# Performance work log

Hardware: AMD Instinct MI355X
Metric: run time of the kernel (lower is better)

## Reference

```python
import jax, jax.numpy as jnp
import numpy as np

B, SEQ, D = 4, 1024, 1024
H = 16
HD = D // H            # 64, matches cos/sin last dim
S_COLS, TOPK = 8, 2
INTER = 768            # find_multiple(round(1.0 * D * 2 / 3), 256)
EPS = 1e-5


def setup_inputs() -> dict:
    key = jax.random.key(0)
    ks = jax.random.split(key, 6)
    hidden_states = jax.random.normal(ks[0], (B, SEQ, D), jnp.float32)
    # RoPE tables (standard rotary, theta=10000)
    inv_freq = 1.0 / (10000.0 ** (jnp.arange(0, HD, 2, dtype=jnp.float32) / HD))
    freqs = jnp.outer(jnp.arange(SEQ, dtype=jnp.float32), inv_freq)
    emb = jnp.concatenate([freqs, freqs], axis=-1)  # [SEQ, HD]
    cos, sin = jnp.cos(emb), jnp.sin(emb)
    Wr = jax.random.normal(ks[1], (S_COLS, D), jnp.float32) * 0.02
    temperature = jnp.ones((1,), jnp.float32)
    # Stacked per-column TransformerBlock params (bias-free linears)
    Wqkv = jax.random.normal(ks[2], (S_COLS, D, 3 * D), jnp.float32) * 0.02
    Wo = jax.random.normal(ks[3], (S_COLS, D, D), jnp.float32) * 0.02
    Wgu = jax.random.normal(ks[4], (S_COLS, D, 2 * INTER), jnp.float32) * 0.02
    Wd = jax.random.normal(ks[5], (S_COLS, INTER, D), jnp.float32) * 0.02
    return dict(hidden_states=hidden_states, cos=cos, sin=sin, Wr=Wr,
                temperature=temperature, Wqkv=Wqkv, Wo=Wo, Wgu=Wgu, Wd=Wd)


def _rms_norm(x):
    return x * jax.lax.rsqrt(jnp.mean(x * x, axis=-1, keepdims=True) + EPS)


def _rotate_half(x):
    x1, x2 = jnp.split(x, 2, axis=-1)
    return jnp.concatenate([-x2, x1], axis=-1)


def _columns_forward(x, Wqkv, Wo, Wgu, Wd, cos, sin):
    # x: [n, seq, D] dispatched sequences; params gathered per dispatch entry [n, ...]
    n, seq, d = x.shape
    qkv = jnp.einsum('nsd,nde->nse', x, Wqkv)
    q, k, v = jnp.split(qkv, 3, axis=-1)
    q = q.reshape(n, seq, H, HD)
    k = k.reshape(n, seq, H, HD)
    v = v.reshape(n, seq, H, HD)
    c = cos[None, :, None, :]
    s = sin[None, :, None, :]
    q = q * c + _rotate_half(q) * s
    k = k * c + _rotate_half(k) * s
    scores = jnp.einsum('nqhd,nkhd->nhqk', q, k) / jnp.sqrt(jnp.asarray(HD, x.dtype))
    attn = jax.nn.softmax(scores, axis=-1)  # non-causal (HRM-style block)
    ctx = jnp.einsum('nhqk,nkhd->nqhd', attn, v).reshape(n, seq, d)
    attn_out = jnp.einsum('nsd,nde->nse', ctx, Wo)
    x = _rms_norm(x + attn_out)                      # post-norm residual
    gu = jnp.einsum('nsd,nde->nse', x, Wgu)
    gate, up = jnp.split(gu, 2, axis=-1)
    mlp_out = jnp.einsum('nsi,nid->nsd', jax.nn.silu(gate) * up, Wd)
    return _rms_norm(x + mlp_out)


def reference(hidden_states, cos, sin, Wr, temperature, Wqkv, Wo, Wgu, Wd):
    Bn = hidden_states.shape[0]
    temp = jnp.clip(temperature, 0.1, 10.0)
    routing_logits = (hidden_states.mean(axis=1) @ Wr.T) / temp   # [B, S]
    topk_vals, topk_idx = jax.lax.top_k(routing_logits, TOPK)
    weights = jax.nn.softmax(topk_vals, axis=-1)                  # [B, k]
    flat_idx = topk_idx.reshape(-1)                               # [B*k] expert ids
    flat_w = weights.reshape(-1)
    sample_idx = jnp.repeat(jnp.arange(Bn), TOPK)                 # [B*k]
    # Sparse dispatch: exactly B*k block forwards via per-entry param gather
    x_disp = hidden_states[sample_idx]
    col_out = _columns_forward(x_disp, Wqkv[flat_idx], Wo[flat_idx],
                               Wgu[flat_idx], Wd[flat_idx], cos, sin)
    result = jnp.zeros_like(hidden_states).at[sample_idx].add(
        flat_w[:, None, None] * col_out)
    return result, routing_logits
```

## Files before the change

### kernel.cpp

```cpp
#include <hip/hip_runtime.h>
#include <hip/hip_bf16.h>
#include <math.h>

#define B_     4
#define SEQ_   1024
#define D_     1024
#define H_     16
#define NE_    8
#define INTER_ 768
#define EPS_   1e-5f

typedef unsigned short u16;
typedef __attribute__((ext_vector_type(8))) short s8v;
typedef __attribute__((ext_vector_type(4))) short s4v;
typedef __attribute__((ext_vector_type(4))) float f4v;
typedef __attribute__((ext_vector_type(4))) unsigned short u16x4;
typedef __attribute__((ext_vector_type(8))) unsigned short u16x8;

__device__ __forceinline__ u16 f2bf(float x) {
    union { float f; unsigned u; } c; c.f = x;
    unsigned r = (c.u + 0x7FFFu + ((c.u >> 16) & 1u)) >> 16;
    return (u16)r;
}
__device__ __forceinline__ float bf2f(u16 h) {
    union { unsigned u; float f; } c; c.u = ((unsigned)h) << 16;
    return c.f;
}
__device__ __forceinline__ unsigned pk2(float a, float b) {
    union { float f; unsigned u; } x, y; x.f = a; y.f = b;
    return ((x.u + 0x8000u) >> 16) | ((y.u + 0x8000u) & 0xffff0000u);
}

#define GLDS16(gp, lp) \
    __builtin_amdgcn_global_load_lds((const __attribute__((address_space(1))) unsigned int*)(gp), \
                                     (__attribute__((address_space(3))) unsigned int*)(lp), 16, 0, 0)

__global__ void route1(const float* __restrict__ hidden, float* __restrict__ part,
                       u16* __restrict__ hb) {
    int b = blockIdx.x, ch = blockIdx.y, t = threadIdx.x;
    const float* xb = hidden + (size_t)b * SEQ_ * D_ + (size_t)ch * 32 * D_;
    u16* ho = hb + (size_t)b * SEQ_ * D_ + (size_t)ch * 32 * D_;
    float4 acc = make_float4(0.f, 0.f, 0.f, 0.f);
    for (int r = 0; r < 32; ++r) {
        float4 v = *(const float4*)&xb[(size_t)r * D_ + t * 4];
        acc.x += v.x; acc.y += v.y; acc.z += v.z; acc.w += v.w;
        u16x4 o = {f2bf(v.x), f2bf(v.y), f2bf(v.z), f2bf(v.w)};
        *(u16x4*)&ho[(size_t)r * D_ + t * 4] = o;
    }
    *(float4*)&part[((size_t)(b * 32 + ch)) * D_ + t * 4] = acc;
}

__global__ void route2(const float* __restrict__ part, const float* __restrict__ Wr,
                       const float* __restrict__ temp, float* __restrict__ out_logits,
                       int* __restrict__ flat_idx, float* __restrict__ flat_w) {
    __shared__ float col[1024];
    __shared__ float sm[8];
    int b = blockIdx.x, t = threadIdx.x;
    float4 s = make_float4(0.f, 0.f, 0.f, 0.f);
    for (int ch = 0; ch < 32; ++ch) {
        float4 v = *(const float4*)&part[((size_t)(b * 32 + ch)) * D_ + t * 4];
        s.x += v.x; s.y += v.y; s.z += v.z; s.w += v.w;
    }
    col[t * 4 + 0] = s.x * (1.f / 1024.f);
    col[t * 4 + 1] = s.y * (1.f / 1024.f);
    col[t * 4 + 2] = s.z * (1.f / 1024.f);
    col[t * 4 + 3] = s.w * (1.f / 1024.f);
    __syncthreads();
    int j = t >> 5, d0 = t & 31;
    float p = 0.f;
    for (int d = d0; d < 1024; d += 32) p += col[d] * Wr[j * 1024 + d];
    for (int off = 16; off >= 1; off >>= 1) p += __shfl_down(p, off, 32);
    if (d0 == 0) sm[j] = p;
    __syncthreads();
    if (t == 0) {
        float tc = temp[0];
        tc = fminf(fmaxf(tc, 0.1f), 10.0f);
        float lg[8];
        for (int jj = 0; jj < 8; ++jj) {
            lg[jj] = sm[jj] / tc;
            out_logits[b * 8 + jj] = lg[jj];
        }
        int i0 = 0; float v0 = lg[0];
        for (int jj = 1; jj < 8; ++jj) if (lg[jj] > v0) { v0 = lg[jj]; i0 = jj; }
        int i1 = -1; float v1 = -1e30f;
        for (int jj = 0; jj < 8; ++jj) if (jj != i0 && lg[jj] > v1) { v1 = lg[jj]; i1 = jj; }
        float e1 = expf(v1 - v0);
        flat_idx[2 * b]     = i0;
        flat_idx[2 * b + 1] = i1;
        flat_w[2 * b]       = 1.0f / (1.0f + e1);
        flat_w[2 * b + 1]   = e1 / (1.0f + e1);
    }
}

__global__ __launch_bounds__(256) void wtrans_all(const float* __restrict__ Wqkv,
                                                  const float* __restrict__ Wo,
                                                  const float* __restrict__ Wgu,
                                                  const float* __restrict__ Wd,
                                                  u16* __restrict__ WqkvT, u16* __restrict__ WoT,
                                                  u16* __restrict__ WguT, u16* __restrict__ WdT) {
    int bid = blockIdx.x;
    const float* W; u16* Wt; int K, N, nx, gu = 0;
    if (bid < 6144)      { W = Wqkv; Wt = WqkvT; K = 1024; N = 3072; nx = 48; }
    else if (bid < 8192) { bid -= 6144;  W = Wo;  Wt = WoT;  K = 1024; N = 1024; nx = 16; }
    else if (bid < 11264){ bid -= 8192;  W = Wgu; Wt = WguT; K = 1024; N = 1536; nx = 24; gu = 1; }
    else                 { bid -= 11264; W = Wd;  Wt = WdT;  K = 768;  N = 1024; nx = 16; }
    int x = bid % nx; bid /= nx;
    int ny = K >> 6;
    int y = bid % ny;
    int e = bid / ny;

    __shared__ float tile[64][65];
    int k0 = y * 64, n0 = x * 64;
    const float* Wp = W + (size_t)e * K * N;
    u16* Wtp = Wt + (size_t)e * K * N;
    int t = threadIdx.x;
    int kk = t >> 4, ns = t & 15;
#pragma unroll
    for (int p = 0; p < 4; ++p) {
        float4 v = *(const float4*)&Wp[(size_t)(k0 + kk + p * 16) * N + n0 + ns * 4];
        tile[kk + p * 16][ns * 4 + 0] = v.x;
        tile[kk + p * 16][ns * 4 + 1] = v.y;
        tile[kk + p * 16][ns * 4 + 2] = v.z;
        tile[kk + p * 16][ns * 4 + 3] = v.w;
    }
    __syncthreads();
    int nn = t >> 3, ks = t & 7;
#pragma unroll
    for (int p = 0; p < 2; ++p) {
        int n = n0 + nn + p * 32;
        int nd = n;
        if (gu) nd = (n < 768) ? ((n >> 4) << 5) + (n & 15)
                               : (((n - 768) >> 4) << 5) + 16 + (n & 15);
        u16x8 o;
#pragma unroll
        for (int jj = 0; jj < 8; ++jj) o[jj] = f2bf(tile[ks * 8 + jj][nn + p * 32]);
        *(u16x8*)&Wtp[(size_t)nd * K + k0 + ks * 8] = o;
    }
}

#define GEMM_CORE(A, Wt, K)                                                                 \
    f4v acc[4][4];                                                                          \
    _Pragma("unroll") for (int i = 0; i < 4; ++i)                                           \
        _Pragma("unroll") for (int jj = 0; jj < 4; ++jj) acc[i][jj] = (f4v){0.f,0.f,0.f,0.f}; \
    for (int k0 = 0; k0 < K; k0 += 32) {                                                    \
        _Pragma("unroll") for (int it = 0; it < 2; ++it) {                                  \
            int p = it * 256 + w * 64 + lane;                                               \
            int row = p >> 2, seg = (p & 3) ^ ((row >> 1) & 3);                             \
            GLDS16(A  + (size_t)(m0 + row) * K + k0 + seg * 8, As + (size_t)(it*256 + w*64) * 8); \
            GLDS16(Wt + (size_t)(n0 + row) * K + k0 + seg * 8, Bs + (size_t)(it*256 + w*64) * 8); \
        }                                                                                   \
        __syncthreads();                                                                    \
        s8v af[4], bfr[4];                                                                  \
        _Pragma("unroll") for (int ti = 0; ti < 4; ++ti) {                                  \
            int r = wm + ti * 16 + c;                                                       \
            af[ti]  = *(const s8v*)&As[r * 32 + (g ^ ((r >> 1) & 3)) * 8];                   \
        }                                                                                   \
        _Pragma("unroll") for (int tj = 0; tj < 4; ++tj) {                                  \
            int r = wn + tj * 16 + c;                                                       \
            bfr[tj] = *(const s8v*)&Bs[r * 32 + (g ^ ((r >> 1) & 3)) * 8];                   \
        }                                                                                   \
        _Pragma("unroll") for (int ti = 0; ti < 4; ++ti)                                    \
            _Pragma("unroll") for (int tj = 0; tj < 4; ++tj)                                \
                acc[ti][tj] = __builtin_amdgcn_mfma_f32_16x16x32_bf16(af[ti], bfr[tj], acc[ti][tj], 0, 0, 0); \
        __syncthreads();                                                                    \
    }

__global__ __launch_bounds__(256) void gemm_bf16(const u16* __restrict__ Abase,
                                                 const u16* __restrict__ Wtbase,
                                                 u16* __restrict__ Cb,
                                                 const int* __restrict__ flat_idx,
                                                 int M, int N, int K, int aDiv) {
    __shared__ __align__(16) u16 As[128 * 32];
    __shared__ __align__(16) u16 Bs[128 * 32];
    int e = blockIdx.z;
    const u16* A  = Abase + (size_t)(e / aDiv) * M * K;
    const u16* Wt = Wtbase + (size_t)flat_idx[e] * N * K;
    int m0 = blockIdx.y * 128, n0 = blockIdx.x * 128;
    int t = threadIdx.x, lane = t & 63, w = t >> 6;
    int g = lane >> 4, c = lane & 15;
    int wm = (w >> 1) * 64, wn = (w & 1) * 64;

    GEMM_CORE(A, Wt, K)

    u16* C = Cb + (size_t)e * M * N;
#pragma unroll
    for (int ti = 0; ti < 4; ++ti)
#pragma unroll
        for (int tj = 0; tj < 4; ++tj)
#pragma unroll
            for (int i = 0; i < 4; ++i)
                C[(size_t)(m0 + wm + ti * 16 + g * 4 + i) * N + n0 + wn + tj * 16 + c] = f2bf(acc[ti][tj][i]);
}

__global__ __launch_bounds__(256) void gemm_qkv(const u16* __restrict__ Abase,
                                                const u16* __restrict__ Wtbase,
                                                const int* __restrict__ flat_idx,
                                                const float* __restrict__ cosb,
                                                const float* __restrict__ sinb,
                                                u16* __restrict__ Qb, u16* __restrict__ Kb,
                                                u16* __restrict__ Vb) {
    __shared__ __align__(16) u16 As[128 * 32];
    __shared__ __align__(16) u16 Bs[128 * 32];
    const int K = 1024, N = 3072;
    int e = blockIdx.z;
    const u16* A  = Abase + (size_t)(e >> 1) * 1024 * K;
    const u16* Wt = Wtbase + (size_t)flat_idx[e] * N * K;
    int m0 = blockIdx.y * 128, n0 = blockIdx.x * 128;
    int t = threadIdx.x, lane = t & 63, w = t >> 6;
    int g = lane >> 4, c = lane & 15;
    int wm = (w >> 1) * 64, wn = (w & 1) * 64;

    GEMM_CORE(A, Wt, K)

    int col0 = n0 + wn;
    int sb = m0 + wm + g * 4;
    if (col0 < 2048) {
        bool isq = col0 < 1024;
        u16* dst = isq ? Qb : Kb;
        int h = (col0 & 1023) >> 6;
        const float scl = isq ? 0.125f * 1.44269504f : 1.0f;
#pragma unroll
        for (int ti = 0; ti < 4; ++ti)
#pragma unroll
            for (int i = 0; i < 4; ++i) {
                int s = sb + ti * 16 + i;
                size_t ob = ((size_t)(e * 1024) + s) * 1024 + h * 64;
#pragma unroll
                for (int tj = 0; tj < 2; ++tj) {
                    int d = tj * 16 + c;
                    float x1 = acc[ti][tj][i], x2 = acc[ti][tj + 2][i];
                    float c1 = cosb[s * 64 + d],      s1 = sinb[s * 64 + d];
                    float c2 = cosb[s * 64 + d + 32], s2 = sinb[s * 64 + d + 32];
                    dst[ob + d]      = f2bf((x1 * c1 - x2 * s1) * scl);
                    dst[ob + d + 32] = f2bf((x2 * c2 + x1 * s2) * scl);
                }
            }
    } else {
        int vcol = col0 - 2048;
#pragma unroll
        for (int ti = 0; ti < 4; ++ti)
#pragma unroll
            for (int tj = 0; tj < 4; ++tj)
#pragma unroll
                for (int i = 0; i < 4; ++i)
                    Vb[((size_t)(e * 1024) + sb + ti * 16 + i) * 1024 + vcol + tj * 16 + c] = f2bf(acc[ti][tj][i]);
    }
}

__global__ __launch_bounds__(256) void gemm_wgu_silu(const u16* __restrict__ Abase,
                                                     const u16* __restrict__ Wtbase,
                                                     u16* __restrict__ act,
                                                     const int* __restrict__ flat_idx) {
    __shared__ __align__(16) u16 As[128 * 32];
    __shared__ __align__(16) u16 Bs[128 * 32];
    const int K = 1024, N = 1536;
    int e = blockIdx.z;
    const u16* A  = Abase + (size_t)e * 1024 * K;
    const u16* Wt = Wtbase + (size_t)flat_idx[e] * N * K;
    int m0 = blockIdx.y * 128, n0 = blockIdx.x * 128;
    int t = threadIdx.x, lane = t & 63, w = t >> 6;
    int g = lane >> 4, c = lane & 15;
    int wm = (w >> 1) * 64, wn = (w & 1) * 64;

    GEMM_CORE(A, Wt, K)

    int col0 = n0 + wn;
    int oc0 = (col0 >> 1) + c;
    int sb = m0 + wm + g * 4;
#pragma unroll
    for (int ti = 0; ti < 4; ++ti)
#pragma unroll
        for (int i = 0; i < 4; ++i) {
            size_t rb = ((size_t)(e * 1024) + sb + ti * 16 + i) * 768;
#pragma unroll
            for (int pr = 0; pr < 2; ++pr) {
                float gt = acc[ti][pr * 2][i];
                float up = acc[ti][pr * 2 + 1][i];
                act[rb + oc0 + pr * 16] = f2bf(gt / (1.f + __expf(-gt)) * up);
            }
        }
}

__global__ __launch_bounds__(256) void vtrans(const u16* __restrict__ Vb, u16* __restrict__ Vtg) {
    __shared__ __align__(16) u16 tile[64 * 72];
    int s0 = blockIdx.x * 64;
    int eh = blockIdx.y;
    int e = eh >> 4, h = eh & 15;
    int t = threadIdx.x;
#pragma unroll
    for (int it = 0; it < 2; ++it) {
        int p = it * 256 + t;
        int sr = p >> 3, ds = p & 7;
        u16x8 v = *(const u16x8*)&Vb[((size_t)(e * 1024) + s0 + sr) * 1024 + h * 64 + ds * 8];
        *(u16x8*)&tile[sr * 72 + ds * 8] = v;
    }
    __syncthreads();
#pragma unroll
    for (int it = 0; it < 2; ++it) {
        int p = it * 256 + t;
        int d = p >> 3, ks = p & 7;
        u16x8 o;
#pragma unroll
        for (int jj = 0; jj < 8; ++jj) o[jj] = tile[(ks * 8 + jj) * 72 + d];
        *(u16x8*)&Vtg[((size_t)((e * 16 + h) * 64) + d) * 1024 + s0 + ks * 8] = o;
    }
}

__global__ __launch_bounds__(256) void attn_mfma(const u16* __restrict__ Qb, const u16* __restrict__ Kb,
                                                 const u16* __restrict__ Vtg, u16* __restrict__ ctx) {
    __shared__ __align__(16) u16 Ks[64 * 64];
    __shared__ __align__(16) u16 Vt[64 * 64];
    int e = blockIdx.x, h = blockIdx.y, qt = blockIdx.z;
    int t = threadIdx.x, lane = t & 63, w = t >> 6;
    int g = lane >> 4, c = lane & 15;
    int q0 = qt * 64 + w * 16;

    s8v qf[2];
#pragma unroll
    for (int ks = 0; ks < 2; ++ks)
        qf[ks] = *(const s8v*)&Qb[((size_t)(e * 1024) + q0 + c) * 1024 + h * 64 + ks * 32 + g * 8];

    f4v O[4];
#pragma unroll
    for (int tj = 0; tj < 4; ++tj) O[tj] = (f4v){0.f, 0.f, 0.f, 0.f};
    f4v liacc = (f4v){0.f, 0.f, 0.f, 0.f};
    const s4v vone = {(short)0x3F80, (short)0x3F80, (short)0x3F80, (short)0x3F80};

    for (int kt = 0; kt < 16; ++kt) {
#pragma unroll
        for (int it = 0; it < 2; ++it) {
            int p = it * 256 + w * 64 + lane;
            int row = p >> 3, ss = p & 7;
            GLDS16(Kb + ((size_t)(e * 1024 + kt * 64 + row)) * 1024 + h * 64 + (ss ^ (row & 7)) * 8,
                   Ks + (size_t)(it * 256 + w * 64) * 8);
            GLDS16(Vtg + ((size_t)((e * 16 + h) * 64 + row)) * 1024 + kt * 64 + (ss ^ (row & 7)) * 8,
                   Vt + (size_t)(it * 256 + w * 64) * 8);
        }
        __syncthreads();

        f4v st[4];
#pragma unroll
        for (int tj = 0; tj < 4; ++tj) st[tj] = (f4v){0.f, 0.f, 0.f, 0.f};
#pragma unroll
        for (int ks = 0; ks < 2; ++ks)
#pragma unroll
            for (int tj = 0; tj < 4; ++tj) {
                int kvl = tj * 16 + c;
                s8v kf = *(const s8v*)&Ks[kvl * 64 + (((ks * 4 + g) ^ (kvl & 7)) * 8)];
                st[tj] = __builtin_amdgcn_mfma_f32_16x16x32_bf16(kf, qf[ks], st[tj], 0, 0, 0);
            }

        s4v pf[4];
#pragma unroll
        for (int tj = 0; tj < 4; ++tj) {
            float p0 = __builtin_amdgcn_exp2f(st[tj][0]);
            float p1 = __builtin_amdgcn_exp2f(st[tj][1]);
            float p2 = __builtin_amdgcn_exp2f(st[tj][2]);
            float p3 = __builtin_amdgcn_exp2f(st[tj][3]);
            union { unsigned u[2]; s4v v; } pu;
            pu.u[0] = pk2(p0, p1);
            pu.u[1] = pk2(p2, p3);
            pf[tj] = pu.v;
        }

#pragma unroll
        for (int tjC = 0; tjC < 4; ++tjC) {
            liacc = __builtin_amdgcn_mfma_f32_16x16x16bf16_1k(pf[tjC], vone, liacc, 0, 0, 0);
#pragma unroll
            for (int tjd = 0; tjd < 4; ++tjd) {
                int d = tjd * 16 + c;
                int sd = tjC * 2 + (g >> 1);
                s4v vf = *(const s4v*)&Vt[d * 64 + ((sd ^ (d & 7)) * 8) + (g & 1) * 4];
                O[tjd] = __builtin_amdgcn_mfma_f32_16x16x16bf16_1k(pf[tjC], vf, O[tjd], 0, 0, 0);
            }
        }
        __syncthreads();
    }
#pragma unroll
    for (int i = 0; i < 4; ++i) {
        float linv = 1.0f / liacc[i];
        size_t rbase = ((size_t)(e * 1024) + q0 + g * 4 + i) * 1024 + h * 64;
#pragma unroll
        for (int tjd = 0; tjd < 4; ++tjd)
            ctx[rbase + tjd * 16 + c] = f2bf(O[tjd][i] * linv);
    }
}

__global__ void add_rmsnorm(const u16* __restrict__ hb, const u16* __restrict__ aob,
                            u16* __restrict__ xnb) {
    int row = blockIdx.x;
    int e = row >> 10;
    int b = e >> 1;
    int s = row & 1023;
    const u16* xr = hb + (((size_t)b * SEQ_ + s) << 10);
    const u16* ar = aob + ((size_t)row << 10);
    u16* o = xnb + ((size_t)row << 10);
    int t = threadIdx.x;
    u16x4 xv = *(const u16x4*)&xr[t * 4];
    u16x4 av = *(const u16x4*)&ar[t * 4];
    float v[4];
    float ss = 0.f;
#pragma unroll
    for (int i = 0; i < 4; ++i) {
        v[i] = bf2f(xv[i]) + bf2f(av[i]);
        ss += v[i] * v[i];
    }
    for (int off = 32; off >= 1; off >>= 1) ss += __shfl_down(ss, off, 64);
    __shared__ float wred[4];
    if ((t & 63) == 0) wred[t >> 6] = ss;
    __syncthreads();
    float tot = wred[0] + wred[1] + wred[2] + wred[3];
    float scale = rsqrtf(tot * (1.0f / 1024.0f) + EPS_);
    u16x4 ov;
#pragma unroll
    for (int i = 0; i < 4; ++i) ov[i] = f2bf(v[i] * scale);
    *(u16x4*)&o[t * 4] = ov;
}

__global__ void final_kernel(const u16* __restrict__ xnb, const u16* __restrict__ mlpb,
                             const float* __restrict__ flat_w, float* __restrict__ out) {
    int row = blockIdx.x;
    int b = row >> 10;
    int s = row & 1023;
    int t = threadIdx.x;
    __shared__ float wred[4];
    float res[4] = {0.f, 0.f, 0.f, 0.f};
    for (int j = 0; j < 2; ++j) {
        int e = 2 * b + j;
        size_t off = (((size_t)e * SEQ_ + s) << 10);
        u16x4 xv = *(const u16x4*)&xnb[off + t * 4];
        u16x4 mv = *(const u16x4*)&mlpb[off + t * 4];
        float v[4];
        float ss = 0.f;
#pragma unroll
        for (int i = 0; i < 4; ++i) {
            v[i] = bf2f(xv[i]) + bf2f(mv[i]);
            ss += v[i] * v[i];
        }
        for (int off2 = 32; off2 >= 1; off2 >>= 1) ss += __shfl_down(ss, off2, 64);
        if ((t & 63) == 0) wred[t >> 6] = ss;
        __syncthreads();
        float tot = wred[0] + wred[1] + wred[2] + wred[3];
        float scale = rsqrtf(tot * (1.0f / 1024.0f) + EPS_);
        float wgt = flat_w[e];
#pragma unroll
        for (int i = 0; i < 4; ++i) res[i] += wgt * v[i] * scale;
        __syncthreads();
    }
    float* o = out + ((size_t)row << 10);
    *(float4*)&o[t * 4] = make_float4(res[0], res[1], res[2], res[3]);
}

extern "C" void kernel_launch(void* const* d_in, const int* in_sizes, int n_in,
                              void* d_out, int out_size, void* d_ws, size_t ws_size,
                              hipStream_t stream) {
    const float* hidden = (const float*)d_in[0];
    const float* cosb   = (const float*)d_in[1];
    const float* sinb   = (const float*)d_in[2];
    const float* Wr     = (const float*)d_in[3];
    const float* temp   = (const float*)d_in[4];
    const float* Wqkv   = (const float*)d_in[5];
    const float* Wo     = (const float*)d_in[6];
    const float* Wgu    = (const float*)d_in[7];
    const float* Wd     = (const float*)d_in[8];
    float* out = (float*)d_out;
    float* out_logits = out + (size_t)B_ * SEQ_ * D_;

    char* base = (char*)d_ws;
    int*   flat_idx = (int*)base;
    float* flat_w   = (float*)(base + 128);
    float* routeP   = (float*)(base + 4096);
    size_t off = (size_t)1 << 20;
    u16* WqkvT = (u16*)(base + off); off += (size_t)8 * 3072 * 1024 * 2;
    u16* WoT   = (u16*)(base + off); off += (size_t)8 * 1024 * 1024 * 2;
    u16* WguT  = (u16*)(base + off); off += (size_t)8 * 1536 * 1024 * 2;
    u16* WdT   = (u16*)(base + off); off += (size_t)8 * 1024 * 768 * 2;
    u16* hb    = (u16*)(base + off); off += (size_t)4 * 1024 * 1024 * 2;
    u16* Qb    = (u16*)(base + off); off += (size_t)8 * 1024 * 1024 * 2;
    u16* Kb    = (u16*)(base + off); off += (size_t)8 * 1024 * 1024 * 2;
    u16* Vb    = (u16*)(base + off); off += (size_t)8 * 1024 * 1024 * 2;
    u16* Vtg   = (u16*)(base + off); off += (size_t)8 * 1024 * 1024 * 2;
    u16* ctxb  = (u16*)(base + off); off += (size_t)8 * 1024 * 1024 * 2;
    u16* aob   = (u16*)(base + off); off += (size_t)8 * 1024 * 1024 * 2;
    u16* xnb   = (u16*)(base + off); off += (size_t)8 * 1024 * 1024 * 2;
    u16* actb  = (u16*)(base + off); off += (size_t)8 * 1024 * 768 * 2;
    u16* mlpb  = (u16*)(base + off); off += (size_t)8 * 1024 * 1024 * 2;

    route1<<<dim3(4, 32), 256, 0, stream>>>(hidden, routeP, hb);
    route2<<<4, 256, 0, stream>>>(routeP, Wr, temp, out_logits, flat_idx, flat_w);
    wtrans_all<<<12800, 256, 0, stream>>>(Wqkv, Wo, Wgu, Wd, WqkvT, WoT, WguT, WdT);

    gemm_qkv<<<dim3(24, 8, 8), 256, 0, stream>>>(hb, WqkvT, flat_idx, cosb, sinb, Qb, Kb, Vb);
    vtrans<<<dim3(16, 128), 256, 0, stream>>>(Vb, Vtg);
    attn_mfma<<<dim3(8, 16, 16), 256, 0, stream>>>(Qb, Kb, Vtg, ctxb);
    gemm_bf16<<<dim3(8, 8, 8), 256, 0, stream>>>(ctxb, WoT, aob, flat_idx, 1024, 1024, 1024, 1);
    add_rmsnorm<<<NE_ * SEQ_, 256, 0, stream>>>(hb, aob, xnb);
    gemm_wgu_silu<<<dim3(12, 8, 8), 256, 0, stream>>>(xnb, WguT, actb, flat_idx);
    gemm_bf16<<<dim3(8, 8, 8), 256, 0, stream>>>(actb, WdT, mlpb, flat_idx, 1024, 1024, 768, 1);
    final_kernel<<<B_ * SEQ_, 256, 0, stream>>>(xnb, mlpb, flat_w, out);
}
```

Before: 545.3 us.

## Skip transposing unused expert weights and use double-buffered 256x256 GEMM tiles

The weight transpose kernel now exits early for experts that no routed entry uses, so it only converts about 8 of 8 experts when they are all selected and fewer otherwise. All GEMMs move from 128x128 tiles with K=32 steps to 256x256 tiles with 512 threads, K=64 steps, double-buffered LDS staging with prefetch of the next tile, an XOR swizzle and setprio around the MFMA bursts. The larger tiles raise operand reuse and hide load latency, but they cut the block count (e.g. 128 blocks for the Wo GEMM) and use 128KB of LDS per block, which may leave the GPU underfilled.

```diff
diff --git a/kernel.cpp b/kernel.cpp
--- a/kernel.cpp
+++ b/kernel.cpp
@@ -97,7 +97,8 @@
                                                   const float* __restrict__ Wgu,
                                                   const float* __restrict__ Wd,
                                                   u16* __restrict__ WqkvT, u16* __restrict__ WoT,
-                                                  u16* __restrict__ WguT, u16* __restrict__ WdT) {
+                                                  u16* __restrict__ WguT, u16* __restrict__ WdT,
+                                                  const int* __restrict__ flat_idx) {
     int bid = blockIdx.x;
     const float* W; u16* Wt; int K, N, nx, gu = 0;
     if (bid < 6144)      { W = Wqkv; Wt = WqkvT; K = 1024; N = 3072; nx = 48; }
@@ -109,6 +110,11 @@
     int y = bid % ny;
     int e = bid / ny;
 
+    bool used = false;
+#pragma unroll
+    for (int jj = 0; jj < 8; ++jj) used |= (flat_idx[jj] == e);
+    if (!used) return;
+
     __shared__ float tile[64][65];
     int k0 = y * 64, n0 = x * 64;
     const float* Wp = W + (size_t)e * K * N;
@@ -138,97 +144,115 @@
     }
 }
 
-#define GEMM_CORE(A, Wt, K)                                                                 \
-    f4v acc[4][4];                                                                          \
-    _Pragma("unroll") for (int i = 0; i < 4; ++i)                                           \
-        _Pragma("unroll") for (int jj = 0; jj < 4; ++jj) acc[i][jj] = (f4v){0.f,0.f,0.f,0.f}; \
-    for (int k0 = 0; k0 < K; k0 += 32) {                                                    \
-        _Pragma("unroll") for (int it = 0; it < 2; ++it) {                                  \
-            int p = it * 256 + w * 64 + lane;                                               \
-            int row = p >> 2, seg = (p & 3) ^ ((row >> 1) & 3);                             \
-            GLDS16(A  + (size_t)(m0 + row) * K + k0 + seg * 8, As + (size_t)(it*256 + w*64) * 8); \
-            GLDS16(Wt + (size_t)(n0 + row) * K + k0 + seg * 8, Bs + (size_t)(it*256 + w*64) * 8); \
-        }                                                                                   \
-        __syncthreads();                                                                    \
-        s8v af[4], bfr[4];                                                                  \
-        _Pragma("unroll") for (int ti = 0; ti < 4; ++ti) {                                  \
-            int r = wm + ti * 16 + c;                                                       \
-            af[ti]  = *(const s8v*)&As[r * 32 + (g ^ ((r >> 1) & 3)) * 8];                   \
-        }                                                                                   \
-        _Pragma("unroll") for (int tj = 0; tj < 4; ++tj) {                                  \
-            int r = wn + tj * 16 + c;                                                       \
-            bfr[tj] = *(const s8v*)&Bs[r * 32 + (g ^ ((r >> 1) & 3)) * 8];                   \
-        }                                                                                   \
-        _Pragma("unroll") for (int ti = 0; ti < 4; ++ti)                                    \
-            _Pragma("unroll") for (int tj = 0; tj < 4; ++tj)                                \
-                acc[ti][tj] = __builtin_amdgcn_mfma_f32_16x16x32_bf16(af[ti], bfr[tj], acc[ti][tj], 0, 0, 0); \
-        __syncthreads();                                                                    \
-    }
-
-__global__ __launch_bounds__(256) void gemm_bf16(const u16* __restrict__ Abase,
-                                                 const u16* __restrict__ Wtbase,
-                                                 u16* __restrict__ Cb,
-                                                 const int* __restrict__ flat_idx,
-                                                 int M, int N, int K, int aDiv) {
-    __shared__ __align__(16) u16 As[128 * 32];
-    __shared__ __align__(16) u16 Bs[128 * 32];
+#define STAGE256(Ap, Wp, Kv, kt, tbv)                                                     \
+    {                                                                                     \
+        const u16* ga_ = (Ap) + (size_t)(m0 + srow) * (Kv) + (kt) * 64 + segsw;           \
+        const u16* gb_ = (Wp) + (size_t)(n0 + srow) * (Kv) + (kt) * 64 + segsw;           \
+        _Pragma("unroll") for (int q_ = 0; q_ < 4; ++q_) {                                \
+            GLDS16(ga_ + (size_t)(q_ * 64) * (Kv), As + (tbv) + q_ * 4096 + w * 512);     \
+            GLDS16(gb_ + (size_t)(q_ * 64) * (Kv), Bs + (tbv) + q_ * 4096 + w * 512);     \
+        }                                                                                 \
+    }
+
+#define COMPUTE256(tbv)                                                                   \
+    _Pragma("unroll") for (int ks_ = 0; ks_ < 2; ++ks_) {                                 \
+        s8v af_[8];                                                                       \
+        int sgk_ = ks_ ? sg1 : sg0;                                                       \
+        _Pragma("unroll") for (int m_ = 0; m_ < 8; ++m_)                                  \
+            af_[m_] = *(const s8v*)&As[(tbv) + rdA + m_ * 1024 + sgk_];                   \
+        _Pragma("unroll") for (int np_ = 0; np_ < 2; ++np_) {                             \
+            s8v b0_ = *(const s8v*)&Bs[(tbv) + rdB + (np_ * 2) * 1024 + sgk_];            \
+            s8v b1_ = *(const s8v*)&Bs[(tbv) + rdB + (np_ * 2 + 1) * 1024 + sgk_];        \
+            __builtin_amdgcn_s_setprio(1);                                                \
+            _Pragma("unroll") for (int m_ = 0; m_ < 8; ++m_) {                            \
+                acc[m_][np_ * 2]     = __builtin_amdgcn_mfma_f32_16x16x32_bf16(af_[m_], b0_, acc[m_][np_ * 2], 0, 0, 0);     \
+                acc[m_][np_ * 2 + 1] = __builtin_amdgcn_mfma_f32_16x16x32_bf16(af_[m_], b1_, acc[m_][np_ * 2 + 1], 0, 0, 0); \
+            }                                                                             \
+            __builtin_amdgcn_s_setprio(0);                                                \
+        }                                                                                 \
+    }
+
+#define GEMM_CORE256(Ap, Wp, Kv)                                                          \
+    __shared__ __align__(16) u16 As[2 * 256 * 64];                                        \
+    __shared__ __align__(16) u16 Bs[2 * 256 * 64];                                        \
+    int t = threadIdx.x, lane = t & 63, w = t >> 6;                                       \
+    int g = lane >> 4, c = lane & 15;                                                     \
+    int wr = w >> 2, wc = w & 3;                                                          \
+    int srow = t >> 3;                                                                    \
+    int segsw = ((t & 7) ^ (srow & 7)) * 8;                                               \
+    int rdA = (wr * 128 + c) * 64;                                                        \
+    int rdB = (wc * 64 + c) * 64;                                                         \
+    int sg0 = (g ^ (c & 7)) * 8, sg1 = ((4 + g) ^ (c & 7)) * 8;                           \
+    f4v acc[8][4];                                                                        \
+    _Pragma("unroll") for (int m_ = 0; m_ < 8; ++m_)                                      \
+        _Pragma("unroll") for (int n_ = 0; n_ < 4; ++n_) acc[m_][n_] = (f4v){0.f, 0.f, 0.f, 0.f}; \
+    const int NT = (Kv) / 64;                                                             \
+    STAGE256(Ap, Wp, Kv, 0, 0)                                                            \
+    __syncthreads();                                                                      \
+    int tb = 0;                                                                           \
+    for (int kt_ = 0; kt_ < NT; ++kt_) {                                                  \
+        if (kt_ + 1 < NT) { STAGE256(Ap, Wp, Kv, kt_ + 1, tb ^ 16384) }                   \
+        COMPUTE256(tb)                                                                    \
+        __syncthreads();                                                                  \
+        tb ^= 16384;                                                                      \
+    }
+
+__global__ __launch_bounds__(512, 2) void gemm_bf16(const u16* __restrict__ Abase,
+                                                    const u16* __restrict__ Wtbase,
+                                                    u16* __restrict__ Cb,
+                                                    const int* __restrict__ flat_idx,
+                                                    int M, int N, int K, int aDiv) {
     int e = blockIdx.z;
     const u16* A  = Abase + (size_t)(e / aDiv) * M * K;
     const u16* Wt = Wtbase + (size_t)flat_idx[e] * N * K;
-    int m0 = blockIdx.y * 128, n0 = blockIdx.x * 128;
-    int t = threadIdx.x, lane = t & 63, w = t >> 6;
-    int g = lane >> 4, c = lane & 15;
-    int wm = (w >> 1) * 64, wn = (w & 1) * 64;
-
-    GEMM_CORE(A, Wt, K)
+    int m0 = blockIdx.y * 256, n0 = blockIdx.x * 256;
+
+    GEMM_CORE256(A, Wt, K)
 
     u16* C = Cb + (size_t)e * M * N;
-#pragma unroll
-    for (int ti = 0; ti < 4; ++ti)
-#pragma unroll
-        for (int tj = 0; tj < 4; ++tj)
+    int rb = m0 + wr * 128 + g * 4;
+    int cb = n0 + wc * 64 + c;
+#pragma unroll
+    for (int m = 0; m < 8; ++m)
+#pragma unroll
+        for (int n = 0; n < 4; ++n)
 #pragma unroll
             for (int i = 0; i < 4; ++i)
-                C[(size_t)(m0 + wm + ti * 16 + g * 4 + i) * N + n0 + wn + tj * 16 + c] = f2bf(acc[ti][tj][i]);
-}
-
-__global__ __launch_bounds__(256) void gemm_qkv(const u16* __restrict__ Abase,
-                                                const u16* __restrict__ Wtbase,
-                                                const int* __restrict__ flat_idx,
-                                                const float* __restrict__ cosb,
-                                                const float* __restrict__ sinb,
-                                                u16* __restrict__ Qb, u16* __restrict__ Kb,
-                                                u16* __restrict__ Vb) {
-    __shared__ __align__(16) u16 As[128 * 32];
-    __shared__ __align__(16) u16 Bs[128 * 32];
+                C[(size_t)(rb + m * 16 + i) * N + cb + n * 16] = f2bf(acc[m][n][i]);
+}
+
+__global__ __launch_bounds__(512, 2) void gemm_qkv(const u16* __restrict__ Abase,
+                                                   const u16* __restrict__ Wtbase,
+                                                   const int* __restrict__ flat_idx,
+                                                   const float* __restrict__ cosb,
+                                                   const float* __restrict__ sinb,
+                                                   u16* __restrict__ Qb, u16* __restrict__ Kb,
+                                                   u16* __restrict__ Vb) {
     const int K = 1024, N = 3072;
     int e = blockIdx.z;
     const u16* A  = Abase + (size_t)(e >> 1) * 1024 * K;
     const u16* Wt = Wtbase + (size_t)flat_idx[e] * N * K;
-    int m0 = blockIdx.y * 128, n0 = blockIdx.x * 128;
-    int t = threadIdx.x, lane = t & 63, w = t >> 6;
-    int g = lane >> 4, c = lane & 15;
-    int wm = (w >> 1) * 64, wn = (w & 1) * 64;
-
-    GEMM_CORE(A, Wt, K)
-
-    int col0 = n0 + wn;
-    int sb = m0 + wm + g * 4;
+    int m0 = blockIdx.y * 256, n0 = blockIdx.x * 256;
+
+    GEMM_CORE256(A, Wt, K)
+
+    int col0 = n0 + wc * 64;
+    int sb = m0 + wr * 128 + g * 4;
     if (col0 < 2048) {
         bool isq = col0 < 1024;
         u16* dst = isq ? Qb : Kb;
         int h = (col0 & 1023) >> 6;
         const float scl = isq ? 0.125f * 1.44269504f : 1.0f;
 #pragma unroll
-        for (int ti = 0; ti < 4; ++ti)
+        for (int m = 0; m < 8; ++m)
 #pragma unroll
             for (int i = 0; i < 4; ++i) {
-                int s = sb + ti * 16 + i;
+                int s = sb + m * 16 + i;
                 size_t ob = ((size_t)(e * 1024) + s) * 1024 + h * 64;
 #pragma unroll
-                for (int tj = 0; tj < 2; ++tj) {
-                    int d = tj * 16 + c;
-                    float x1 = acc[ti][tj][i], x2 = acc[ti][tj + 2][i];
+                for (int nj = 0; nj < 2; ++nj) {
+                    int d = nj * 16 + c;
+                    float x1 = acc[m][nj][i], x2 = acc[m][nj + 2][i];
                     float c1 = cosb[s * 64 + d],      s1 = sinb[s * 64 + d];
                     float c2 = cosb[s * 64 + d + 32], s2 = sinb[s * 64 + d + 32];
                     dst[ob + d]      = f2bf((x1 * c1 - x2 * s1) * scl);
@@ -238,44 +262,39 @@
     } else {
         int vcol = col0 - 2048;
 #pragma unroll
-        for (int ti = 0; ti < 4; ++ti)
-#pragma unroll
-            for (int tj = 0; tj < 4; ++tj)
+        for (int m = 0; m < 8; ++m)
+#pragma unroll
+            for (int n = 0; n < 4; ++n)
 #pragma unroll
                 for (int i = 0; i < 4; ++i)
-                    Vb[((size_t)(e * 1024) + sb + ti * 16 + i) * 1024 + vcol + tj * 16 + c] = f2bf(acc[ti][tj][i]);
-    }
-}
-
-__global__ __launch_bounds__(256) void gemm_wgu_silu(const u16* __restrict__ Abase,
-                                                     const u16* __restrict__ Wtbase,
-                                                     u16* __restrict__ act,
-                                                     const int* __restrict__ flat_idx) {
-    __shared__ __align__(16) u16 As[128 * 32];
-    __shared__ __align__(16) u16 Bs[128 * 32];
+                    Vb[((size_t)(e * 1024) + sb + m * 16 + i) * 1024 + vcol + n * 16 + c] = f2bf(acc[m][n][i]);
+    }
+}
+
+__global__ __launch_bounds__(512, 2) void gemm_wgu_silu(const u16* __restrict__ Abase,
+                                                        const u16* __restrict__ Wtbase,
+                                                        u16* __restrict__ act,
+                                                        const int* __restrict__ flat_idx) {
     const int K = 1024, N = 1536;
     int e = blockIdx.z;
     const u16* A  = Abase + (size_t)e * 1024 * K;
     const u16* Wt = Wtbase + (size_t)flat_idx[e] * N * K;
-    int m0 = blockIdx.y * 128, n0 = blockIdx.x * 128;
-    int t = threadIdx.x, lane = t & 63, w = t >> 6;
-    int g = lane >> 4, c = lane & 15;
-    int wm = (w >> 1) * 64, wn = (w & 1) * 64;
-
-    GEMM_CORE(A, Wt, K)
-
-    int col0 = n0 + wn;
+    int m0 = blockIdx.y * 256, n0 = blockIdx.x * 256;
+
+    GEMM_CORE256(A, Wt, K)
+
+    int col0 = n0 + wc * 64;
     int oc0 = (col0 >> 1) + c;
-    int sb = m0 + wm + g * 4;
-#pragma unroll
-    for (int ti = 0; ti < 4; ++ti)
+    int sb = m0 + wr * 128 + g * 4;
+#pragma unroll
+    for (int m = 0; m < 8; ++m)
 #pragma unroll
         for (int i = 0; i < 4; ++i) {
-            size_t rb = ((size_t)(e * 1024) + sb + ti * 16 + i) * 768;
+            size_t rb = ((size_t)(e * 1024) + sb + m * 16 + i) * 768;
 #pragma unroll
             for (int pr = 0; pr < 2; ++pr) {
-                float gt = acc[ti][pr * 2][i];
-                float up = acc[ti][pr * 2 + 1][i];
+                float gt = acc[m][pr * 2][i];
+                float up = acc[m][pr * 2 + 1][i];
                 act[rb + oc0 + pr * 16] = f2bf(gt / (1.f + __expf(-gt)) * up);
             }
         }
@@ -488,14 +507,14 @@
 
     route1<<<dim3(4, 32), 256, 0, stream>>>(hidden, routeP, hb);
     route2<<<4, 256, 0, stream>>>(routeP, Wr, temp, out_logits, flat_idx, flat_w);
-    wtrans_all<<<12800, 256, 0, stream>>>(Wqkv, Wo, Wgu, Wd, WqkvT, WoT, WguT, WdT);
-
-    gemm_qkv<<<dim3(24, 8, 8), 256, 0, stream>>>(hb, WqkvT, flat_idx, cosb, sinb, Qb, Kb, Vb);
+    wtrans_all<<<12800, 256, 0, stream>>>(Wqkv, Wo, Wgu, Wd, WqkvT, WoT, WguT, WdT, flat_idx);
+
+    gemm_qkv<<<dim3(12, 4, 8), 512, 0, stream>>>(hb, WqkvT, flat_idx, cosb, sinb, Qb, Kb, Vb);
     vtrans<<<dim3(16, 128), 256, 0, stream>>>(Vb, Vtg);
     attn_mfma<<<dim3(8, 16, 16), 256, 0, stream>>>(Qb, Kb, Vtg, ctxb);
-    gemm_bf16<<<dim3(8, 8, 8), 256, 0, stream>>>(ctxb, WoT, aob, flat_idx, 1024, 1024, 1024, 1);
+    gemm_bf16<<<dim3(4, 4, 8), 512, 0, stream>>>(ctxb, WoT, aob, flat_idx, 1024, 1024, 1024, 1);
     add_rmsnorm<<<NE_ * SEQ_, 256, 0, stream>>>(hb, aob, xnb);
-    gemm_wgu_silu<<<dim3(12, 8, 8), 256, 0, stream>>>(xnb, WguT, actb, flat_idx);
-    gemm_bf16<<<dim3(8, 8, 8), 256, 0, stream>>>(actb, WdT, mlpb, flat_idx, 1024, 1024, 768, 1);
+    gemm_wgu_silu<<<dim3(6, 4, 8), 512, 0, stream>>>(xnb, WguT, actb, flat_idx);
+    gemm_bf16<<<dim3(4, 4, 8), 512, 0, stream>>>(actb, WdT, mlpb, flat_idx, 1024, 1024, 768, 1);
     final_kernel<<<B_ * SEQ_, 256, 0, stream>>>(xnb, mlpb, flat_w, out);
 }
```

After: 525.9 us. 3.5% less time.
